# Kernel tuning notes

Measured on AMD Instinct MI355X. Metric: run time of the kernel, lower is better.

Reference implementation:

```python
import jax, jax.numpy as jnp
import numpy as np

N, C, G, M, E = 100000, 8, 8, 32, 1600000
EPS = 1e-8


def setup_inputs() -> dict:
    key = jax.random.key(0)
    k1, k2, k3, k4, k5 = jax.random.split(key, 5)
    x = jax.random.randint(k1, (N,), 0, M)
    prev_h = jax.random.uniform(k2, (N, C, G), dtype=jnp.float32)
    edge_index = jax.random.randint(k3, (2, E), 0, N)
    Q_neigh = jax.random.normal(k4, (C, C, G), dtype=jnp.float32) * 1.25
    B = jax.random.normal(k5, (C, M, G), dtype=jnp.float32) * 1.25
    return {"x": x, "prev_h": prev_h, "edge_index": edge_index,
            "Q_neigh": Q_neigh, "B": B}


def reference(x, prev_h, edge_index, Q_neigh, B):
    n = prev_h.shape[0]
    # softmax reparameterization (vectorized over n_gen)
    Qs = jax.nn.softmax(Q_neigh, axis=0)          # [C, C, G], columns sum to 1 over dim 0
    Bs = jax.nn.softmax(B, axis=1)                # [C, M, G], rows sum to 1 over M

    dst, src = edge_index[0], edge_index[1]
    neigh = prev_h[src]                            # [E, C, G] gather
    summed = jax.ops.segment_sum(neigh, dst, num_segments=n)            # [N, C, G]
    counts = jax.ops.segment_sum(jnp.ones((src.shape[0],), prev_h.dtype), dst,
                                 num_segments=n)                        # [N]
    aggr = summed / jnp.maximum(counts, 1.0)[:, None, None]             # scatter-mean, 0 for isolated nodes

    B_nodes = jnp.transpose(Bs[:, x], (1, 0, 2))[:, :, None, :]         # [N, C, 1, G]
    unnorm = B_nodes * (Qs[None, :, :, :] * aggr[:, None, :, :]) + EPS  # [N, C, C, G]

    denom = unnorm.sum(axis=(1, 2), keepdims=True)                      # [N, 1, 1, G]
    posterior_il = unnorm / denom
    posterior_i = posterior_il.sum(axis=2)                              # [N, C, G]
    likelihood = jnp.log(jnp.squeeze(denom, (1, 2)))                    # [N, G]
    return likelihood, posterior_i
```

## Files before the change

### kernel.cpp

```cpp
#include <hip/hip_runtime.h>

#define C_    8
#define G_    8
#define CG    64
#define CAP   48
#define CELL  56
#define BSPAN 256
#define SBLK  256
#define CVT   160
#define BG    512
#define Z1    2048
#define Z2    2048
#define ZTOT  4096
#define EPSF  1e-8f

__device__ __forceinline__ unsigned short bf16rne(float v) {
    unsigned u = __float_as_uint(v);
    return (unsigned short)((u + 0x7FFFu + ((u >> 16) & 1u)) >> 16);
}
__device__ __forceinline__ float bf16tof(unsigned short h) {
    return __uint_as_float((unsigned)h << 16);
}

__device__ __forceinline__ void zsum_block(int zgid, const float* __restrict__ Bmat,
                                           float* __restrict__ Z, int M) {
    if (zgid >= ZTOT) return;
    __shared__ float zpart[4][8];
    int c = zgid & 7, bx = zgid >> 3;
    const float4* B4 = (const float4*)(Bmat + (size_t)c * M * G_);
    const int total4 = M * 2;
    int tid = bx * 256 + threadIdx.x;
    const int zstride = (ZTOT / 8) * 256;
    float a0 = 0.f, a1 = 0.f, a2 = 0.f, a3 = 0.f;
    for (int f = tid; f < total4; f += zstride) {
        float4 v = B4[f];
        a0 += __expf(v.x); a1 += __expf(v.y); a2 += __expf(v.z); a3 += __expf(v.w);
    }
    #pragma unroll
    for (int m = 2; m <= 32; m <<= 1) {
        a0 += __shfl_xor(a0, m, 64);
        a1 += __shfl_xor(a1, m, 64);
        a2 += __shfl_xor(a2, m, 64);
        a3 += __shfl_xor(a3, m, 64);
    }
    int lane = threadIdx.x & 63, w = threadIdx.x >> 6;
    if (lane < 2) {
        int g0 = lane * 4;
        zpart[w][g0 + 0] = a0; zpart[w][g0 + 1] = a1;
        zpart[w][g0 + 2] = a2; zpart[w][g0 + 3] = a3;
    }
    __syncthreads();
    if (threadIdx.x < 8) {
        float s = zpart[0][threadIdx.x] + zpart[1][threadIdx.x]
                + zpart[2][threadIdx.x] + zpart[3][threadIdx.x];
        atomicAdd(&Z[c * G_ + threadIdx.x], s);
    }
}

__global__ void k_d1(const int* __restrict__ ei, int E, int npart,
                     int* __restrict__ counts, int* __restrict__ staging,
                     const float* __restrict__ prev_h, unsigned short* __restrict__ ph16,
                     int N, const float* __restrict__ Qn, float* __restrict__ Qs,
                     const int* __restrict__ x, unsigned short* __restrict__ blog16,
                     const float* __restrict__ Bmat, float* __restrict__ Z, int M) {
    int b = blockIdx.x;
    if (b < SBLK) {
        __shared__ int cur[512];
        for (int p = threadIdx.x; p < npart; p += 256) cur[p] = 0;
        __syncthreads();
        int chunk = (E + SBLK - 1) / SBLK;
        int lo = b * chunk, hi = min(E, lo + chunk);
        for (int e = lo + threadIdx.x; e < hi; e += 256) {
            int dst = ei[e], src = ei[E + e];
            int p = dst >> 8;
            int c = atomicAdd(&cur[p], 1);
            if (c < CELL) staging[(p * SBLK + b) * CELL + c] = ((dst & 255) << 23) | src;
        }
        __syncthreads();
        for (int p = threadIdx.x; p < npart; p += 256)
            counts[p * SBLK + b] = cur[p];
    } else if (b < SBLK + CVT) {
        int gid = (b - SBLK) * 256 + threadIdx.x;
        int total8 = N * 8;
        const int cstride = CVT * 256;
        for (int f = gid; f < total8; f += cstride) {
            const float4* s = (const float4*)(prev_h + (size_t)f * 8);
            float4 v0 = s[0], v1 = s[1];
            float vv[8] = {v0.x, v0.y, v0.z, v0.w, v1.x, v1.y, v1.z, v1.w};
            unsigned r[4];
            #pragma unroll
            for (int k = 0; k < 4; ++k)
                r[k] = (unsigned)bf16rne(vv[2 * k]) | ((unsigned)bf16rne(vv[2 * k + 1]) << 16);
            *(uint4*)(ph16 + (size_t)f * 8) = make_uint4(r[0], r[1], r[2], r[3]);
        }
        if (b == SBLK && threadIdx.x < 64)
            ph16[(size_t)N * CG + threadIdx.x] = 0;
    } else if (b == SBLK + CVT) {
        __shared__ float e[512];
        __shared__ float cs[64];
        int t = threadIdx.x;
        e[t] = __expf(Qn[t]); e[t + 256] = __expf(Qn[t + 256]);
        __syncthreads();
        if (t < 64) {
            float s = 0.f;
            #pragma unroll
            for (int i2 = 0; i2 < 8; ++i2) s += e[i2 * 64 + t];
            cs[t] = s;
        }
        __syncthreads();
        Qs[t] = e[t] / cs[t & 63];
        Qs[t + 256] = e[t + 256] / cs[t & 63];
    } else if (b < SBLK + CVT + 1 + BG) {
        int gidx = b - (SBLK + CVT + 1);
        int lane = threadIdx.x & 63, w = threadIdx.x >> 6;
        int i = lane >> 3, g = lane & 7;
        const int step = BG * 4 * 4;
        for (int n0 = (gidx * 4 + w) * 4; n0 < N; n0 += step) {
            int xs[4];
            #pragma unroll
            for (int k = 0; k < 4; ++k) xs[k] = (n0 + k < N) ? x[n0 + k] : 0;
            #pragma unroll
            for (int k = 0; k < 4; ++k)
                if (n0 + k < N)
                    blog16[(size_t)(n0 + k) * CG + lane] =
                        bf16rne(Bmat[((size_t)i * M + xs[k]) * G_ + g]);
        }
    } else {
        zsum_block(b - (SBLK + CVT + 1 + BG), Bmat, Z, M);
    }
}

__global__ void k_d2(const int* __restrict__ counts, const int* __restrict__ staging,
                     int* __restrict__ cnt, int* __restrict__ csr, int N, int npart,
                     const float* __restrict__ Bmat, float* __restrict__ Z, int M) {
    int b = blockIdx.x;
    if (b >= npart) { zsum_block(Z1 + (b - npart), Bmat, Z, M); return; }
    __shared__ int cl[BSPAN];
    __shared__ int csl[BSPAN * CAP];
    int t = threadIdx.x;
    cl[t] = 0;
    __syncthreads();
    int cnum = min(counts[b * SBLK + t], CELL);
    int cbase = (b * SBLK + t) * CELL;
    for (int j = 0; j < cnum; ++j) {
        int v = staging[cbase + j];
        int local = (unsigned)v >> 23;
        int src = v & 0x7FFFFF;
        int pos = atomicAdd(&cl[local], 1);
        if (pos < CAP) csl[local * CAP + pos] = src;
    }
    __syncthreads();
    int n = b * BSPAN + t;
    if (n < N) cnt[n] = cl[t];
    for (int idx = t; idx < BSPAN * CAP; idx += 256) {
        int local = idx / CAP, pos = idx - local * CAP;
        csr[(size_t)b * (BSPAN * CAP) + idx] =
            (pos < min(cl[local], CAP)) ? csl[idx] : N;
    }
}

__global__ void __launch_bounds__(128)
k_ti(const unsigned short* __restrict__ ph16, const int* __restrict__ cnt,
     const int* __restrict__ csr, const float* __restrict__ Qs,
     const unsigned short* __restrict__ blog16,
     const float* __restrict__ Z, float* __restrict__ out, int N) {
    int lane = threadIdx.x & 63, w = threadIdx.x >> 6;
    int i = lane >> 3, g = lane & 7;
    int base = blockIdx.x * 8 + w * 4;
    if (base >= N) return;
    float invZ = 1.f / Z[lane];
    int nk[4]; bool valid[4]; int deg[4], ng[4];
    #pragma unroll
    for (int k = 0; k < 4; ++k) {
        int n = base + k;
        valid[k] = (n < N);
        nk[k] = valid[k] ? n : (N - 1);
    }
    #pragma unroll
    for (int k = 0; k < 4; ++k) {
        deg[k] = valid[k] ? cnt[nk[k]] : 0;
        ng[k]  = (min(deg[k], CAP) + 3) >> 2;
    }
    float q[8];
    #pragma unroll
    for (int l = 0; l < 8; ++l) q[l] = Qs[i * 64 + l * 8 + g];
    const unsigned short* phl = ph16 + lane;
    float acc[4] = {0.f, 0.f, 0.f, 0.f};
    int ngmax = max(max(ng[0], ng[1]), max(ng[2], ng[3]));
    #pragma unroll 2
    for (int q2 = 0; q2 < ngmax; ++q2) {
        int4 s4[4];
        #pragma unroll
        for (int k = 0; k < 4; ++k) {
            int idx = min(q2, ng[k] > 0 ? ng[k] - 1 : 0);
            s4[k] = ((const int4*)(csr + (size_t)nk[k] * CAP))[q2 < ng[k] ? q2 : (CAP / 4 - 1)];
        }
        #pragma unroll
        for (int k = 0; k < 4; ++k) {
            acc[k] += bf16tof(phl[(size_t)s4[k].x << 6]);
            acc[k] += bf16tof(phl[(size_t)s4[k].y << 6]);
            acc[k] += bf16tof(phl[(size_t)s4[k].z << 6]);
            acc[k] += bf16tof(phl[(size_t)s4[k].w << 6]);
        }
    }
    #pragma unroll
    for (int k = 0; k < 4; ++k) {
        float aggr = (deg[k] > 0) ? acc[k] / (float)deg[k] : 0.f;
        float ti = 0.f;
        #pragma unroll
        for (int l = 0; l < 8; ++l) ti += q[l] * __shfl(aggr, l * 8 + g, 64);
        float bl = bf16tof(blog16[(size_t)nk[k] * CG + lane]);
        float u = __expf(bl) * invZ * ti;
        float s = u;
        #pragma unroll
        for (int m = 8; m <= 32; m <<= 1) s += __shfl_xor(s, m, 64);
        float denom = s + 64.f * EPSF;
        if (valid[k]) {
            if (i == 0) out[nk[k] * G_ + g] = logf(denom);
            out[(size_t)N * G_ + (size_t)nk[k] * CG + lane] = (u + 8.f * EPSF) / denom;
        }
    }
}

extern "C" void kernel_launch(void* const* d_in, const int* in_sizes, int n_in,
                              void* d_out, int out_size, void* d_ws, size_t ws_size,
                              hipStream_t stream) {
    const int*   x      = (const int*)d_in[0];
    const float* prev_h = (const float*)d_in[1];
    const int*   ei     = (const int*)d_in[2];
    const float* Qn     = (const float*)d_in[3];
    const float* Bm     = (const float*)d_in[4];
    float* out = (float*)d_out;

    int N = in_sizes[0];
    int E = in_sizes[2] / 2;
    int M = in_sizes[4] / CG;
    int npart = (N + BSPAN - 1) / BSPAN;

    float* Z      = (float*)d_ws;
    float* Qs     = Z + 64;
    int*   counts = (int*)d_ws + 576;
    int*   cnt    = counts + npart * SBLK;
    int*   stag   = cnt + N;
    int*   csr    = stag + (size_t)npart * SBLK * CELL;
    unsigned short* ph16   = (unsigned short*)(csr + (size_t)npart * BSPAN * CAP);
    unsigned short* blog16 = ph16 + (size_t)(N + 1) * CG;

    hipMemsetAsync(d_ws, 0, 64 * sizeof(float), stream);

    k_d1<<<SBLK + CVT + 1 + BG + Z1, 256, 0, stream>>>(
        ei, E, npart, counts, stag, prev_h, ph16, N, Qn, Qs, x, blog16, Bm, Z, M);
    k_d2<<<npart + Z2, 256, 0, stream>>>(counts, stag, cnt, csr, N, npart, Bm, Z, M);
    k_ti<<<(N + 7) / 8, 128, 0, stream>>>(ph16, cnt, csr, Qs, blog16, Z, out, N);
}
```

Before: 139.4 us.

## Overlap Z normalizer reduction with aggregation and split epilogue kernel

```diff
diff --git a/kernel.cpp b/kernel.cpp
--- a/kernel.cpp
+++ b/kernel.cpp
@@ -9,8 +9,8 @@
 #define SBLK  256
 #define CVT   160
 #define BG    512
-#define Z1    2048
-#define Z2    2048
+#define Z1    1024
+#define Z2    512
 #define ZTOT  4096
 #define EPSF  1e-8f
 
@@ -159,16 +159,17 @@
     }
 }
 
-__global__ void __launch_bounds__(128)
-k_ti(const unsigned short* __restrict__ ph16, const int* __restrict__ cnt,
-     const int* __restrict__ csr, const float* __restrict__ Qs,
-     const unsigned short* __restrict__ blog16,
-     const float* __restrict__ Z, float* __restrict__ out, int N) {
+__global__ void k_ti(const unsigned short* __restrict__ ph16, const int* __restrict__ cnt,
+                     const int* __restrict__ csr, const float* __restrict__ Qs,
+                     unsigned short* __restrict__ ti16,
+                     const float* __restrict__ Bmat, float* __restrict__ Z,
+                     int M, int N) {
+    int grp = blockIdx.x / 5, r = blockIdx.x % 5;
+    if (r >= 3) { zsum_block(Z1 + Z2 + grp * 2 + (r - 3), Bmat, Z, M); return; }
     int lane = threadIdx.x & 63, w = threadIdx.x >> 6;
     int i = lane >> 3, g = lane & 7;
-    int base = blockIdx.x * 8 + w * 4;
+    int base = (grp * 3 + r) * 16 + w * 4;
     if (base >= N) return;
-    float invZ = 1.f / Z[lane];
     int nk[4]; bool valid[4]; int deg[4], ng[4];
     #pragma unroll
     for (int k = 0; k < 4; ++k) {
@@ -191,10 +192,8 @@
     for (int q2 = 0; q2 < ngmax; ++q2) {
         int4 s4[4];
         #pragma unroll
-        for (int k = 0; k < 4; ++k) {
-            int idx = min(q2, ng[k] > 0 ? ng[k] - 1 : 0);
-            s4[k] = ((const int4*)(csr + (size_t)nk[k] * CAP))[q2 < ng[k] ? q2 : (CAP / 4 - 1)];
-        }
+        for (int k = 0; k < 4; ++k)
+            s4[k] = ((const int4*)(csr + (size_t)nk[k] * CAP))[q2];
         #pragma unroll
         for (int k = 0; k < 4; ++k) {
             acc[k] += bf16tof(phl[(size_t)s4[k].x << 6]);
@@ -209,16 +208,31 @@
         float ti = 0.f;
         #pragma unroll
         for (int l = 0; l < 8; ++l) ti += q[l] * __shfl(aggr, l * 8 + g, 64);
-        float bl = bf16tof(blog16[(size_t)nk[k] * CG + lane]);
+        if (valid[k]) ti16[(size_t)nk[k] * CG + lane] = bf16rne(ti);
+    }
+}
+
+__global__ void k_epi(const unsigned short* __restrict__ ti16,
+                      const unsigned short* __restrict__ blog16,
+                      const float* __restrict__ Z, float* __restrict__ out, int N) {
+    int w = threadIdx.x >> 6, lane = threadIdx.x & 63;
+    int i = lane >> 3, g = lane & 7;
+    int base = (blockIdx.x * 4 + w) * 4;
+    if (base >= N) return;
+    float invZ = 1.f / Z[lane];
+    #pragma unroll
+    for (int k = 0; k < 4; ++k) {
+        int n = base + k;
+        if (n >= N) break;
+        float ti = bf16tof(ti16[(size_t)n * CG + lane]);
+        float bl = bf16tof(blog16[(size_t)n * CG + lane]);
         float u = __expf(bl) * invZ * ti;
         float s = u;
         #pragma unroll
         for (int m = 8; m <= 32; m <<= 1) s += __shfl_xor(s, m, 64);
         float denom = s + 64.f * EPSF;
-        if (valid[k]) {
-            if (i == 0) out[nk[k] * G_ + g] = logf(denom);
-            out[(size_t)N * G_ + (size_t)nk[k] * CG + lane] = (u + 8.f * EPSF) / denom;
-        }
+        if (i == 0) out[n * G_ + g] = logf(denom);
+        out[(size_t)N * G_ + (size_t)n * CG + lane] = (u + 8.f * EPSF) / denom;
     }
 }
 
@@ -236,6 +250,8 @@
     int E = in_sizes[2] / 2;
     int M = in_sizes[4] / CG;
     int npart = (N + BSPAN - 1) / BSPAN;
+    int nAggr = (N + 15) / 16;
+    int ngroups = (nAggr + 2) / 3;
 
     float* Z      = (float*)d_ws;
     float* Qs     = Z + 64;
@@ -245,11 +261,13 @@
     int*   csr    = stag + (size_t)npart * SBLK * CELL;
     unsigned short* ph16   = (unsigned short*)(csr + (size_t)npart * BSPAN * CAP);
     unsigned short* blog16 = ph16 + (size_t)(N + 1) * CG;
+    unsigned short* ti16   = blog16 + (size_t)N * CG;
 
     hipMemsetAsync(d_ws, 0, 64 * sizeof(float), stream);
 
     k_d1<<<SBLK + CVT + 1 + BG + Z1, 256, 0, stream>>>(
         ei, E, npart, counts, stag, prev_h, ph16, N, Qn, Qs, x, blog16, Bm, Z, M);
     k_d2<<<npart + Z2, 256, 0, stream>>>(counts, stag, cnt, csr, N, npart, Bm, Z, M);
-    k_ti<<<(N + 7) / 8, 128, 0, stream>>>(ph16, cnt, csr, Qs, blog16, Z, out, N);
-}
+    k_ti<<<ngroups * 5, 256, 0, stream>>>(ph16, cnt, csr, Qs, ti16, Bm, Z, M, N);
+    k_epi<<<(N + 15) / 16, 256, 0, stream>>>(ti16, blog16, Z, out, N);
+}
```

Result: faster. 130.5 us (-6.4%).
